# Performance work log

Hardware: AMD Instinct MI355X
Metric: run time of the kernel (lower is better)

Reference implementation:

```python
import jax, jax.numpy as jnp
import numpy as np

B, T, C = 2, 2048, 1024
NH, HD = 16, 64  # n_head, head_dim (qk == vo)


def setup_inputs() -> dict:
    key = jax.random.key(0)
    ks = jax.random.split(key, 5)
    scale = 1.0 / np.sqrt(C)
    return {
        "x": jax.random.normal(ks[0], (B, T, C), dtype=jnp.float32),
        "Wq": jax.random.normal(ks[1], (C, C), dtype=jnp.float32) * scale,
        "Wk": jax.random.normal(ks[2], (C, C), dtype=jnp.float32) * scale,
        "Wv": jax.random.normal(ks[3], (C, C), dtype=jnp.float32) * scale,
        "Wo": jax.random.normal(ks[4], (C, C), dtype=jnp.float32) * scale,
    }


def reference(x, Wq, Wk, Wv, Wo):
    # torch Linear: y = x @ W.T (weights stored [out, in])
    q = (x @ Wq.T).reshape(B, T, NH, HD).transpose(0, 2, 1, 3)  # [B,H,T,D]
    k = (x @ Wk.T).reshape(B, T, NH, HD).transpose(0, 2, 1, 3)
    v = (x @ Wv.T).reshape(B, T, NH, HD).transpose(0, 2, 1, 3)
    att = jnp.einsum("bhqd,bhkd->bhqk", q, k) * (1.0 / np.sqrt(HD))
    causal = jnp.tril(jnp.ones((T, T), dtype=bool))
    att = jnp.where(causal[None, None], att, -jnp.inf)
    att = jax.nn.softmax(att, axis=-1)
    y = jnp.einsum("bhqk,bhkd->bhqd", att, v)  # [B,H,T,D]
    y = y.transpose(0, 2, 1, 3).reshape(B, T, NH * HD)
    return y @ Wo.T  # dropout p=0 -> identity
```

## Files before the change

kernel.cpp:

```cpp
#include <hip/hip_runtime.h>
#include <hip/hip_bf16.h>
#include <cstdint>
#include <cstddef>
#include <cmath>

#define B_  2
#define T_  2048
#define C_  1024
#define NH_ 16
#define HD_ 64

typedef __bf16 bf16;
typedef bf16  bf16x8 __attribute__((ext_vector_type(8)));
typedef bf16  bf16x4 __attribute__((ext_vector_type(4)));
typedef float f32x4  __attribute__((ext_vector_type(4)));

#define MFMA16(a, b, c) __builtin_amdgcn_mfma_f32_16x16x32_bf16((a), (b), (c), 0, 0, 0)

__device__ __forceinline__ void gld_lds16(const bf16* g, bf16* lds_base_uniform) {
    __builtin_amdgcn_global_load_lds(
        (const __attribute__((address_space(1))) uint32_t*)g,
        (__attribute__((address_space(3))) uint32_t*)lds_base_uniform,
        16, 0, 0);
}

__global__ __launch_bounds__(256) void cast_all(const float* __restrict__ x,
                                                const float* __restrict__ Wq,
                                                const float* __restrict__ Wk,
                                                const float* __restrict__ Wv,
                                                const float* __restrict__ Wo,
                                                bf16* __restrict__ xb,
                                                bf16* __restrict__ Wqk,
                                                bf16* __restrict__ Wvb,
                                                bf16* __restrict__ Wob) {
    const int bid = blockIdx.x;
    if (bid < 4096) {
        const int i = bid * 256 + threadIdx.x;
        float4 v = ((const float4*)x)[i];
        ((bf16x4*)xb)[i] = bf16x4{ (bf16)v.x, (bf16)v.y, (bf16)v.z, (bf16)v.w };
    } else {
        const float C1 = 0.1803368801111f;
        const int i = (bid - 4096) * 256 + threadIdx.x;
        const int nw4 = C_ * C_ / 4;
        float4 q = ((const float4*)Wq)[i];
        float4 k = ((const float4*)Wk)[i];
        float4 v = ((const float4*)Wv)[i];
        float4 o = ((const float4*)Wo)[i];
        ((bf16x4*)Wqk)[i]       = bf16x4{ (bf16)(q.x * C1), (bf16)(q.y * C1),
                                          (bf16)(q.z * C1), (bf16)(q.w * C1) };
        ((bf16x4*)Wqk)[nw4 + i] = bf16x4{ (bf16)k.x, (bf16)k.y, (bf16)k.z, (bf16)k.w };
        ((bf16x4*)Wvb)[i]       = bf16x4{ (bf16)v.x, (bf16)v.y, (bf16)v.z, (bf16)v.w };
        ((bf16x4*)Wob)[i]       = bf16x4{ (bf16)o.x, (bf16)o.y, (bf16)o.z, (bf16)o.w };
    }
}

__device__ __forceinline__ void gemm_tile(bf16* As, bf16* Bs,
                                          const bf16* __restrict__ A,
                                          const bf16* __restrict__ W,
                                          bf16* __restrict__ Y,
                                          int N, int K, int m0, int n0) {
    const int tid  = threadIdx.x;
    const int lane = tid & 63;
    const int w    = tid >> 6;
    const int ml   = lane & 15;
    const int quad = lane >> 4;
    const int wm   = (w >> 1) * 64;
    const int wn   = (w & 1) * 64;
    const int sr   = lane >> 2;
    const int sc   = lane & 3;

    f32x4 acc[4][4] = {};

    for (int k0 = 0; k0 < K; k0 += 32) {
        __syncthreads();
#pragma unroll
        for (int ei = 0; ei < 2; ++ei) {
            const int e = w * 2 + ei;
            gld_lds16(A + (size_t)(m0 + e * 16 + sr) * K + k0 + sc * 8, &As[e * 512]);
            gld_lds16(W + (size_t)(n0 + e * 16 + sr) * K + k0 + sc * 8, &Bs[e * 512]);
        }
        __builtin_amdgcn_s_waitcnt(0);
        __syncthreads();

        bf16x8 af[4], bfr[4];
#pragma unroll
        for (int t = 0; t < 4; ++t) {
            af[t]  = *(const bf16x8*)&As[(wm + t * 16 + ml) * 32 + quad * 8];
            bfr[t] = *(const bf16x8*)&Bs[(wn + t * 16 + ml) * 32 + quad * 8];
        }
#pragma unroll
        for (int mt = 0; mt < 4; ++mt)
#pragma unroll
            for (int nt = 0; nt < 4; ++nt)
                acc[mt][nt] = MFMA16(af[mt], bfr[nt], acc[mt][nt]);
    }

#pragma unroll
    for (int mt = 0; mt < 4; ++mt)
#pragma unroll
        for (int nt = 0; nt < 4; ++nt)
#pragma unroll
            for (int r = 0; r < 4; ++r) {
                const int row = m0 + wm + mt * 16 + quad * 4 + r;
                const int col = n0 + wn + nt * 16 + ml;
                Y[(size_t)row * N + col] = (bf16)acc[mt][nt][r];
            }
}

__global__ __launch_bounds__(256) void proj_fused(const bf16* __restrict__ xb,
                                                  const bf16* __restrict__ Wqk,
                                                  const bf16* __restrict__ Wvb,
                                                  bf16* __restrict__ QKb,
                                                  bf16* __restrict__ VtT) {
    __shared__ __align__(16) bf16 As[128 * 32];
    __shared__ __align__(16) bf16 Bs[128 * 32];
    const int bid = blockIdx.x;
    if (bid < 512) {
        gemm_tile(As, Bs, xb, Wqk, QKb, 2048, 1024, (bid >> 4) * 128, (bid & 15) * 128);
    } else {
        const int b2 = bid - 512;
        gemm_tile(As, Bs, Wvb, xb, VtT, 4096, 1024, (b2 >> 5) * 128, (b2 & 31) * 128);
    }
}

__global__ __launch_bounds__(256) void gemm_wo(const bf16* __restrict__ A,
                                               const bf16* __restrict__ W,
                                               float* __restrict__ Y) {
    __shared__ __align__(16) bf16 As[64 * 32];
    __shared__ __align__(16) bf16 Bs[128 * 32];
    const int tid  = threadIdx.x;
    const int lane = tid & 63;
    const int w    = tid >> 6;
    const int ml   = lane & 15;
    const int quad = lane >> 4;
    const int wm   = (w >> 1) * 32;
    const int wn   = (w & 1) * 64;
    const int m0   = blockIdx.y * 64;
    const int n0   = blockIdx.x * 128;
    const int sr   = lane >> 2;
    const int sc   = lane & 3;

    f32x4 acc[2][4] = {};

    for (int k0 = 0; k0 < 1024; k0 += 32) {
        __syncthreads();
        gld_lds16(A + (size_t)(m0 + w * 16 + sr) * 1024 + k0 + sc * 8, &As[w * 512]);
#pragma unroll
        for (int ei = 0; ei < 2; ++ei) {
            const int e = w * 2 + ei;
            gld_lds16(W + (size_t)(n0 + e * 16 + sr) * 1024 + k0 + sc * 8, &Bs[e * 512]);
        }
        __builtin_amdgcn_s_waitcnt(0);
        __syncthreads();

        bf16x8 af[2], bfr[4];
#pragma unroll
        for (int t = 0; t < 2; ++t)
            af[t] = *(const bf16x8*)&As[(wm + t * 16 + ml) * 32 + quad * 8];
#pragma unroll
        for (int t = 0; t < 4; ++t)
            bfr[t] = *(const bf16x8*)&Bs[(wn + t * 16 + ml) * 32 + quad * 8];
#pragma unroll
        for (int mt = 0; mt < 2; ++mt)
#pragma unroll
            for (int nt = 0; nt < 4; ++nt)
                acc[mt][nt] = MFMA16(af[mt], bfr[nt], acc[mt][nt]);
    }

#pragma unroll
    for (int mt = 0; mt < 2; ++mt)
#pragma unroll
        for (int nt = 0; nt < 4; ++nt)
#pragma unroll
            for (int r = 0; r < 4; ++r) {
                const int row = m0 + wm + mt * 16 + quad * 4 + r;
                const int col = n0 + wn + nt * 16 + ml;
                Y[(size_t)row * 1024 + col] = acc[mt][nt][r];
            }
}

__global__ __launch_bounds__(256, 4) void attn_mfma(const bf16* __restrict__ QKb,
                                                    const bf16* __restrict__ VtT,
                                                    bf16* __restrict__ Pbuf,
                                                    float* __restrict__ Lbuf) {
    const int bid  = blockIdx.x;
    const int hb   = bid & 31;
    const int s    = 79 - (bid >> 5);
    int qt, chunk;
    if (s < 8)       { qt = s;                   chunk = 0; }
    else if (s < 24) { qt = 8  + ((s - 8) >> 1); chunk = (s - 8) & 1; }
    else if (s < 48) { qt = 16 + (s - 24) / 3;   chunk = (s - 24) % 3; }
    else             { qt = 24 + ((s - 48) >> 2); chunk = (s - 48) & 3; }
    const int h = hb >> 1, b = hb & 1;

    const int tid  = threadIdx.x;
    const int lane = tid & 63;
    const int w    = tid >> 6;
    const int ml   = lane & 15;
    const int quad = lane >> 4;

    __shared__ __align__(16) bf16 Ks[2][4096];
    __shared__ __align__(16) bf16 Vs[2][4096];
    __shared__ __align__(16) bf16 Ps[4][16 * 64];

    const bf16* Qbase = QKb + (size_t)b * T_ * 2048 + (size_t)h * HD_;
    const bf16* Kbase = Qbase + 1024;
    const bf16* Vbase = VtT + (size_t)h * HD_ * 4096 + (size_t)b * T_;

    const int qrow = qt * 64 + w * 16 + ml;
    bf16x8 qf[2];
#pragma unroll
    for (int ks = 0; ks < 2; ++ks)
        qf[ks] = *(const bf16x8*)(Qbase + (size_t)qrow * 2048 + ks * 32 + quad * 8);

    f32x4 o_acc[4] = {};
    f32x4 l_acc = {};
    bf16x8 onesf;
#pragma unroll
    for (int j = 0; j < 8; ++j) onesf[j] = (bf16)1.0f;

    const int sr = lane >> 2, sc = lane & 3;
    bf16* ps = &Ps[w][0];
    uint16_t* ps16 = (uint16_t*)ps;

    const int ktbase  = chunk * 8;
    const int nrounds = min(8, qt + 1 - ktbase);

    auto stageKV = [&](int ktg, int buf) {
        const int k0 = ktg * 64;
#pragma unroll
        for (int ei = 0; ei < 2; ++ei) {
            const int e = w * 2 + ei;
            const int r = (e & 3) * 16 + sr;
            const int ch = (e >> 2) * 32 + sc * 8;
            gld_lds16(Kbase + (size_t)(k0 + r) * 2048 + ch, &Ks[buf][e * 512]);
            gld_lds16(Vbase + (size_t)r * 4096 + k0 + ch, &Vs[buf][e * 512]);
        }
    };

    auto phase1 = [&](int cur, int ktg) {
        const int k0 = ktg * 64;
#pragma unroll
        for (int nt = 0; nt < 4; ++nt) {
            f32x4 sacc = {};
#pragma unroll
            for (int ks = 0; ks < 2; ++ks) {
                bf16x8 kf = *(const bf16x8*)&Ks[cur][ks * 2048 + (nt * 16 + ml) * 32 + quad * 8];
                sacc = MFMA16(qf[ks], kf, sacc);
            }
            const int kg = k0 + nt * 16 + ml;
#pragma unroll
            for (int r = 0; r < 4; ++r) {
                float arg = sacc[r];
                if (ktg == qt) {
                    const int qg = qt * 64 + w * 16 + quad * 4 + r;
                    if (kg > qg) arg = -1e30f;
                }
                const float p = __builtin_amdgcn_exp2f(arg);
                const int row = quad * 4 + r;
                ps16[row * 64 + ((nt * 16 + ml) ^ ((row & 7) << 3))] =
                    (uint16_t)(__builtin_bit_cast(uint32_t, p) >> 16);
            }
        }
    };

    auto phase2 = [&](int cur) {
#pragma unroll
        for (int ks = 0; ks < 2; ++ks) {
            bf16x8 pf = *(const bf16x8*)&ps[ml * 64 + ((((ks << 2) + quad) ^ (ml & 7)) << 3)];
            l_acc = MFMA16(pf, onesf, l_acc);
#pragma unroll
            for (int nt = 0; nt < 4; ++nt) {
                bf16x8 vf = *(const bf16x8*)&Vs[cur][ks * 2048 + (nt * 16 + ml) * 32 + quad * 8];
                o_acc[nt] = MFMA16(pf, vf, o_acc[nt]);
            }
        }
    };

    stageKV(ktbase, 0);
    asm volatile("s_waitcnt vmcnt(0)" ::: "memory");
    asm volatile("s_barrier" ::: "memory");

    for (int j = 0; j < nrounds; ++j) {
        const int cur = j & 1;
        const int ktg = ktbase + j;

        if (j + 1 < nrounds) stageKV(ktg + 1, cur ^ 1);
        phase1(cur, ktg);
        phase2(cur);
        if (j + 1 < nrounds) {
            asm volatile("s_waitcnt vmcnt(0)" ::: "memory");
            asm volatile("s_barrier" ::: "memory");
        }
    }

    const int slotIdx = hb * 80 + s;
    bf16* pb = Pbuf + (size_t)slotIdx * 4096;
#pragma unroll
    for (int r = 0; r < 4; ++r) {
        const int prow = w * 16 + quad * 4 + r;
#pragma unroll
        for (int nt = 0; nt < 4; ++nt)
            pb[prow * 64 + nt * 16 + ml] = (bf16)o_acc[nt][r];
        if (ml == 0)
            Lbuf[slotIdx * 64 + prow] = l_acc[r];
    }
}

__global__ __launch_bounds__(256) void attn_merge(const bf16* __restrict__ Pbuf,
                                                  const float* __restrict__ Lbuf,
                                                  bf16* __restrict__ Ab) {
    const int gid = blockIdx.x;
    const int qt  = gid >> 5;
    const int hb  = gid & 31;
    const int h = hb >> 1, b = hb & 1;
    int s0;
    if (qt < 8)       s0 = qt;
    else if (qt < 16) s0 = 8 + (qt - 8) * 2;
    else if (qt < 24) s0 = 24 + (qt - 16) * 3;
    else              s0 = 48 + (qt - 24) * 4;
    const int nch = (qt + 8) >> 3;

    const int tid = threadIdx.x;
    const int row = tid >> 2;
    const int cg  = (tid & 3) * 16;

    float acc[16] = {};
    float lsum = 0.f;
    for (int c = 0; c < nch; ++c) {
        const int slotIdx = hb * 80 + s0 + c;
        lsum += Lbuf[slotIdx * 64 + row];
        const bf16* pb = Pbuf + (size_t)slotIdx * 4096 + row * 64 + cg;
        bf16x8 v0 = *(const bf16x8*)pb;
        bf16x8 v1 = *(const bf16x8*)(pb + 8);
#pragma unroll
        for (int j = 0; j < 8; ++j) { acc[j] += (float)v0[j]; acc[8 + j] += (float)v1[j]; }
    }
    const float rcl = 1.0f / lsum;
    bf16x8 o0, o1;
#pragma unroll
    for (int j = 0; j < 8; ++j) { o0[j] = (bf16)(acc[j] * rcl); o1[j] = (bf16)(acc[8 + j] * rcl); }
    bf16* dst = Ab + (size_t)(b * T_ + qt * 64 + row) * 1024 + h * 64 + cg;
    *(bf16x8*)dst = o0;
    *(bf16x8*)(dst + 8) = o1;
}

extern "C" void kernel_launch(void* const* d_in, const int* in_sizes, int n_in,
                              void* d_out, int out_size, void* d_ws, size_t ws_size,
                              hipStream_t stream) {
    const float* x  = (const float*)d_in[0];
    const float* Wq = (const float*)d_in[1];
    const float* Wk = (const float*)d_in[2];
    const float* Wv = (const float*)d_in[3];
    const float* Wo = (const float*)d_in[4];
    float* out = (float*)d_out;

    const size_t n_x = (size_t)B_ * T_ * C_;
    const size_t n_w = (size_t)C_ * C_;

    bf16* xb   = (bf16*)d_ws;
    bf16* Wqk  = xb + n_x;
    bf16* Wvb  = Wqk + 2 * n_w;
    bf16* Wob  = Wvb + n_w;
    bf16* QKb  = Wob + n_w;
    bf16* VtT  = QKb + 2 * n_x;
    bf16* Ab   = VtT + n_x;
    bf16* Pbuf = Ab + n_x;
    float* Lbuf = (float*)(Pbuf + (size_t)2560 * 4096);

    cast_all<<<5120, 256, 0, stream>>>(x, Wq, Wk, Wv, Wo, xb, Wqk, Wvb, Wob);

    proj_fused<<<768, 256, 0, stream>>>(xb, Wqk, Wvb, QKb, VtT);

    attn_mfma<<<2560, 256, 0, stream>>>(QKb, VtT, Pbuf, Lbuf);
    attn_merge<<<1024, 256, 0, stream>>>(Pbuf, Lbuf, Ab);

    gemm_wo<<<dim3(1024 / 128, 4096 / 64), 256, 0, stream>>>(Ab, Wob, out);
}
```

Baseline: 185.9 us.

## Switch attention to 32x32 MFMA with 128-row query tiles and swizzled LDS

The attention kernel now processes 128 query rows per block, 32 per wave, using 32x32x16 bf16 MFMA instead of 16x16x32. This halves the number of blocks and partial slots, so each staged K/V tile is reused by twice as many queries. K/V staging uses an XOR-swizzled LDS layout to cut bank conflicts, and the merge kernel is resized to match. The cost is more accumulator registers (launch bounds lowered from 4 to 3 blocks), coarser work units that can worsen load balance on the causal triangle, and more wasted masked work on diagonal tiles.

```diff
diff --git a/kernel.cpp b/kernel.cpp
--- a/kernel.cpp
+++ b/kernel.cpp
@@ -14,8 +14,10 @@
 typedef bf16  bf16x8 __attribute__((ext_vector_type(8)));
 typedef bf16  bf16x4 __attribute__((ext_vector_type(4)));
 typedef float f32x4  __attribute__((ext_vector_type(4)));
+typedef float f32x16 __attribute__((ext_vector_type(16)));
 
 #define MFMA16(a, b, c) __builtin_amdgcn_mfma_f32_16x16x32_bf16((a), (b), (c), 0, 0, 0)
+#define MFMA32(a, b, c) __builtin_amdgcn_mfma_f32_32x32x16_bf16((a), (b), (c), 0, 0, 0)
 
 __device__ __forceinline__ void gld_lds16(const bf16* g, bf16* lds_base_uniform) {
     __builtin_amdgcn_global_load_lds(
@@ -179,102 +181,107 @@
             }
 }
 
-__global__ __launch_bounds__(256, 4) void attn_mfma(const bf16* __restrict__ QKb,
+__global__ __launch_bounds__(256, 3) void attn_mfma(const bf16* __restrict__ QKb,
                                                     const bf16* __restrict__ VtT,
                                                     bf16* __restrict__ Pbuf,
                                                     float* __restrict__ Lbuf) {
-    const int bid  = blockIdx.x;
-    const int hb   = bid & 31;
-    const int s    = 79 - (bid >> 5);
-    int qt, chunk;
-    if (s < 8)       { qt = s;                   chunk = 0; }
-    else if (s < 24) { qt = 8  + ((s - 8) >> 1); chunk = (s - 8) & 1; }
-    else if (s < 48) { qt = 16 + (s - 24) / 3;   chunk = (s - 24) % 3; }
-    else             { qt = 24 + ((s - 48) >> 2); chunk = (s - 48) & 3; }
+    const int bid = blockIdx.x;
+    const int hb  = bid & 31;
+    const int s   = 39 - (bid >> 5);
+    int it, chunk;
+    if (s < 4)       { it = s;                  chunk = 0; }
+    else if (s < 12) { it = 4 + ((s - 4) >> 1); chunk = (s - 4) & 1; }
+    else if (s < 24) { it = 8 + (s - 12) / 3;   chunk = (s - 12) % 3; }
+    else             { it = 12 + ((s - 24) >> 2); chunk = (s - 24) & 3; }
     const int h = hb >> 1, b = hb & 1;
 
     const int tid  = threadIdx.x;
     const int lane = tid & 63;
     const int w    = tid >> 6;
-    const int ml   = lane & 15;
-    const int quad = lane >> 4;
+    const int keyl = lane & 31;
+    const int hi   = lane >> 5;
 
     __shared__ __align__(16) bf16 Ks[2][4096];
     __shared__ __align__(16) bf16 Vs[2][4096];
-    __shared__ __align__(16) bf16 Ps[4][16 * 64];
+    __shared__ __align__(16) bf16 Ps[4][2048];
 
     const bf16* Qbase = QKb + (size_t)b * T_ * 2048 + (size_t)h * HD_;
     const bf16* Kbase = Qbase + 1024;
     const bf16* Vbase = VtT + (size_t)h * HD_ * 4096 + (size_t)b * T_;
 
-    const int qrow = qt * 64 + w * 16 + ml;
-    bf16x8 qf[2];
-#pragma unroll
-    for (int ks = 0; ks < 2; ++ks)
-        qf[ks] = *(const bf16x8*)(Qbase + (size_t)qrow * 2048 + ks * 32 + quad * 8);
-
-    f32x4 o_acc[4] = {};
-    f32x4 l_acc = {};
+    const int qrow = it * 128 + w * 32 + keyl;
+    bf16x8 qf[4];
+#pragma unroll
+    for (int dc = 0; dc < 4; ++dc)
+        qf[dc] = *(const bf16x8*)(Qbase + (size_t)qrow * 2048 + dc * 16 + hi * 8);
+
+    f32x16 o_acc[2] = {};
+    f32x16 l_acc = {};
     bf16x8 onesf;
 #pragma unroll
     for (int j = 0; j < 8; ++j) onesf[j] = (bf16)1.0f;
 
-    const int sr = lane >> 2, sc = lane & 3;
     bf16* ps = &Ps[w][0];
     uint16_t* ps16 = (uint16_t*)ps;
 
     const int ktbase  = chunk * 8;
-    const int nrounds = min(8, qt + 1 - ktbase);
+    const int nrounds = min(8, 2 * it + 2 - ktbase);
 
     auto stageKV = [&](int ktg, int buf) {
         const int k0 = ktg * 64;
 #pragma unroll
         for (int ei = 0; ei < 2; ++ei) {
-            const int e = w * 2 + ei;
-            const int r = (e & 3) * 16 + sr;
-            const int ch = (e >> 2) * 32 + sc * 8;
-            gld_lds16(Kbase + (size_t)(k0 + r) * 2048 + ch, &Ks[buf][e * 512]);
-            gld_lds16(Vbase + (size_t)r * 4096 + k0 + ch, &Vs[buf][e * 512]);
+            const int e  = w * 2 + ei;
+            const int rr = e * 8 + (lane >> 3);
+            const int g  = (lane & 7) ^ (lane >> 3);
+            gld_lds16(Kbase + (size_t)(k0 + rr) * 2048 + g * 8, &Ks[buf][e * 512]);
+            gld_lds16(Vbase + (size_t)rr * 4096 + k0 + g * 8, &Vs[buf][e * 512]);
         }
     };
 
     auto phase1 = [&](int cur, int ktg) {
         const int k0 = ktg * 64;
-#pragma unroll
-        for (int nt = 0; nt < 4; ++nt) {
-            f32x4 sacc = {};
-#pragma unroll
-            for (int ks = 0; ks < 2; ++ks) {
-                bf16x8 kf = *(const bf16x8*)&Ks[cur][ks * 2048 + (nt * 16 + ml) * 32 + quad * 8];
-                sacc = MFMA16(qf[ks], kf, sacc);
-            }
-            const int kg = k0 + nt * 16 + ml;
-#pragma unroll
-            for (int r = 0; r < 4; ++r) {
+        const bool domask = (k0 + 63) > (it * 128 + w * 32);
+#pragma unroll
+        for (int kh = 0; kh < 2; ++kh) {
+            f32x16 sacc = {};
+#pragma unroll
+            for (int dc = 0; dc < 4; ++dc) {
+                bf16x8 kf = *(const bf16x8*)&Ks[cur][(kh * 32 + keyl) * 64 +
+                                                     ((((dc << 1) | hi)) ^ (keyl & 7)) * 8];
+                sacc = MFMA32(qf[dc], kf, sacc);
+            }
+            const int kg = k0 + kh * 32 + keyl;
+#pragma unroll
+            for (int r = 0; r < 16; ++r) {
                 float arg = sacc[r];
-                if (ktg == qt) {
-                    const int qg = qt * 64 + w * 16 + quad * 4 + r;
+                const int qloc = (r & 3) + 8 * (r >> 2) + 4 * hi;
+                if (domask) {
+                    const int qg = it * 128 + w * 32 + qloc;
                     if (kg > qg) arg = -1e30f;
                 }
                 const float p = __builtin_amdgcn_exp2f(arg);
-                const int row = quad * 4 + r;
-                ps16[row * 64 + ((nt * 16 + ml) ^ ((row & 7) << 3))] =
+                ps16[qloc * 64 + (((kh * 4 + (keyl >> 3)) ^ (qloc & 7)) << 3) + (keyl & 7)] =
                     (uint16_t)(__builtin_bit_cast(uint32_t, p) >> 16);
             }
         }
     };
 
     auto phase2 = [&](int cur) {
-#pragma unroll
-        for (int ks = 0; ks < 2; ++ks) {
-            bf16x8 pf = *(const bf16x8*)&ps[ml * 64 + ((((ks << 2) + quad) ^ (ml & 7)) << 3)];
-            l_acc = MFMA16(pf, onesf, l_acc);
-#pragma unroll
-            for (int nt = 0; nt < 4; ++nt) {
-                bf16x8 vf = *(const bf16x8*)&Vs[cur][ks * 2048 + (nt * 16 + ml) * 32 + quad * 8];
-                o_acc[nt] = MFMA16(pf, vf, o_acc[nt]);
-            }
-        }
+        bf16x8 pa[4];
+#pragma unroll
+        for (int kc = 0; kc < 4; ++kc) {
+            pa[kc] = *(const bf16x8*)&ps[keyl * 64 + (((kc << 1) | hi) ^ (keyl & 7)) * 8];
+            l_acc = MFMA32(pa[kc], onesf, l_acc);
+        }
+#pragma unroll
+        for (int dh = 0; dh < 2; ++dh)
+#pragma unroll
+            for (int kc = 0; kc < 4; ++kc) {
+                bf16x8 vf = *(const bf16x8*)&Vs[cur][(dh * 32 + keyl) * 64 +
+                                                     (((kc << 1) | hi) ^ (keyl & 7)) * 8];
+                o_acc[dh] = MFMA32(pa[kc], vf, o_acc[dh]);
+            }
     };
 
     stageKV(ktbase, 0);
@@ -284,7 +291,6 @@
     for (int j = 0; j < nrounds; ++j) {
         const int cur = j & 1;
         const int ktg = ktbase + j;
-
         if (j + 1 < nrounds) stageKV(ktg + 1, cur ^ 1);
         phase1(cur, ktg);
         phase2(cur);
@@ -294,16 +300,21 @@
         }
     }
 
-    const int slotIdx = hb * 80 + s;
-    bf16* pb = Pbuf + (size_t)slotIdx * 4096;
-#pragma unroll
-    for (int r = 0; r < 4; ++r) {
-        const int prow = w * 16 + quad * 4 + r;
-#pragma unroll
-        for (int nt = 0; nt < 4; ++nt)
-            pb[prow * 64 + nt * 16 + ml] = (bf16)o_acc[nt][r];
-        if (ml == 0)
-            Lbuf[slotIdx * 64 + prow] = l_acc[r];
+    const int slotIdx = hb * 40 + s;
+    bf16* pb = Pbuf + (size_t)slotIdx * 8192;
+#pragma unroll
+    for (int dh = 0; dh < 2; ++dh)
+#pragma unroll
+        for (int r = 0; r < 16; ++r) {
+            const int qloc = w * 32 + (r & 3) + 8 * (r >> 2) + 4 * hi;
+            pb[qloc * 64 + dh * 32 + keyl] = (bf16)o_acc[dh][r];
+        }
+    if (keyl == 0) {
+#pragma unroll
+        for (int r = 0; r < 16; ++r) {
+            const int qloc = w * 32 + (r & 3) + 8 * (r >> 2) + 4 * hi;
+            Lbuf[slotIdx * 128 + qloc] = l_acc[r];
+        }
     }
 }
 
@@ -311,38 +322,42 @@
                                                   const float* __restrict__ Lbuf,
                                                   bf16* __restrict__ Ab) {
     const int gid = blockIdx.x;
-    const int qt  = gid >> 5;
+    const int it  = gid >> 5;
     const int hb  = gid & 31;
     const int h = hb >> 1, b = hb & 1;
     int s0;
-    if (qt < 8)       s0 = qt;
-    else if (qt < 16) s0 = 8 + (qt - 8) * 2;
-    else if (qt < 24) s0 = 24 + (qt - 16) * 3;
-    else              s0 = 48 + (qt - 24) * 4;
-    const int nch = (qt + 8) >> 3;
+    if (it < 4)       s0 = it;
+    else if (it < 8)  s0 = 4 + (it - 4) * 2;
+    else if (it < 12) s0 = 12 + (it - 8) * 3;
+    else              s0 = 24 + (it - 12) * 4;
+    const int nch = (2 * it + 9) >> 3;
 
     const int tid = threadIdx.x;
-    const int row = tid >> 2;
-    const int cg  = (tid & 3) * 16;
-
-    float acc[16] = {};
+    const int row = tid >> 1;
+    const int cg  = (tid & 1) * 32;
+
+    float acc[32] = {};
     float lsum = 0.f;
     for (int c = 0; c < nch; ++c) {
-        const int slotIdx = hb * 80 + s0 + c;
-        lsum += Lbuf[slotIdx * 64 + row];
-        const bf16* pb = Pbuf + (size_t)slotIdx * 4096 + row * 64 + cg;
-        bf16x8 v0 = *(const bf16x8*)pb;
-        bf16x8 v1 = *(const bf16x8*)(pb + 8);
-#pragma unroll
-        for (int j = 0; j < 8; ++j) { acc[j] += (float)v0[j]; acc[8 + j] += (float)v1[j]; }
+        const int slot = hb * 40 + s0 + c;
+        lsum += Lbuf[slot * 128 + row];
+        const bf16* pb = Pbuf + (size_t)slot * 8192 + row * 64 + cg;
+#pragma unroll
+        for (int g = 0; g < 4; ++g) {
+            bf16x8 v = *(const bf16x8*)(pb + g * 8);
+#pragma unroll
+            for (int j = 0; j < 8; ++j) acc[g * 8 + j] += (float)v[j];
+        }
     }
     const float rcl = 1.0f / lsum;
-    bf16x8 o0, o1;
-#pragma unroll
-    for (int j = 0; j < 8; ++j) { o0[j] = (bf16)(acc[j] * rcl); o1[j] = (bf16)(acc[8 + j] * rcl); }
-    bf16* dst = Ab + (size_t)(b * T_ + qt * 64 + row) * 1024 + h * 64 + cg;
-    *(bf16x8*)dst = o0;
-    *(bf16x8*)(dst + 8) = o1;
+    bf16* dst = Ab + (size_t)(b * T_ + it * 128 + row) * 1024 + h * 64 + cg;
+#pragma unroll
+    for (int g = 0; g < 4; ++g) {
+        bf16x8 o;
+#pragma unroll
+        for (int j = 0; j < 8; ++j) o[j] = (bf16)(acc[g * 8 + j] * rcl);
+        *(bf16x8*)(dst + g * 8) = o;
+    }
 }
 
 extern "C" void kernel_launch(void* const* d_in, const int* in_sizes, int n_in,
@@ -366,14 +381,14 @@
     bf16* VtT  = QKb + 2 * n_x;
     bf16* Ab   = VtT + n_x;
     bf16* Pbuf = Ab + n_x;
-    float* Lbuf = (float*)(Pbuf + (size_t)2560 * 4096);
+    float* Lbuf = (float*)(Pbuf + (size_t)1280 * 8192);
 
     cast_all<<<5120, 256, 0, stream>>>(x, Wq, Wk, Wv, Wo, xb, Wqk, Wvb, Wob);
 
     proj_fused<<<768, 256, 0, stream>>>(xb, Wqk, Wvb, QKb, VtT);
 
-    attn_mfma<<<2560, 256, 0, stream>>>(QKb, VtT, Pbuf, Lbuf);
-    attn_merge<<<1024, 256, 0, stream>>>(Pbuf, Lbuf, Ab);
+    attn_mfma<<<1280, 256, 0, stream>>>(QKb, VtT, Pbuf, Lbuf);
+    attn_merge<<<512, 256, 0, stream>>>(Pbuf, Lbuf, Ab);
 
     gemm_wo<<<dim3(1024 / 128, 4096 / 64), 256, 0, stream>>>(Ab, Wob, out);
 }
```

Result: faster. 181.9 us (-2.1%).
